# Kernel tuning notes

Measured on AMD Instinct MI355X. Metric: run time of the kernel, lower is better.

## Reference

```python
import jax, jax.numpy as jnp
import numpy as np

B, T, C = 2, 2048, 2048
N_HEAD, N_GROUP = 32, 8
HEAD_DIM = C // N_HEAD           # 64
HIG = N_HEAD // N_GROUP          # heads per group = 4


def setup_inputs() -> dict:
    key = jax.random.key(0)
    ks = jax.random.split(key, 8)
    s = 1.0 / np.sqrt(C)
    return {
        "q": jax.random.normal(ks[0], (B, T, C), jnp.float32),
        "k": jax.random.normal(ks[1], (B, T, C), jnp.float32),
        "v": jax.random.normal(ks[2], (B, T, C), jnp.float32),
        "Wq": jax.random.normal(ks[3], (C, C), jnp.float32) * s,
        "Wk": jax.random.normal(ks[4], (N_GROUP * HEAD_DIM, C), jnp.float32) * s,
        "Wv": jax.random.normal(ks[5], (N_GROUP * HEAD_DIM, C), jnp.float32) * s,
        "Wp": jax.random.normal(ks[6], (C, C), jnp.float32) * s,
        "bp": jax.random.normal(ks[7], (C,), jnp.float32) * s,
    }


def reference(q, k, v, Wq, Wk, Wv, Wp, bp):
    # Q projection -> (B, HIG, G, T, D); head h = i*G + g (row-major split of n_head)
    qp = (q @ Wq.T).reshape(B, T, N_HEAD, HEAD_DIM)
    qp = qp.transpose(0, 2, 1, 3).reshape(B, HIG, N_GROUP, T, HEAD_DIM)
    # K/V projections -> (B, G, T, D), shared across heads within a group
    kp = (k @ Wk.T).reshape(B, T, N_GROUP, HEAD_DIM).transpose(0, 2, 1, 3)
    vp = (v @ Wv.T).reshape(B, T, N_GROUP, HEAD_DIM).transpose(0, 2, 1, 3)
    scale = 1.0 / jnp.sqrt(jnp.asarray(HEAD_DIM, qp.dtype))
    scores = jnp.einsum('bigtd,bgsd->bigts', qp, kp) * scale  # (B,HIG,G,T,T)
    attn = jax.nn.softmax(scores, axis=-1)
    out = jnp.einsum('bigts,bgsd->bigtd', attn, vp)           # (B,HIG,G,T,D)
    out = out.reshape(B, N_HEAD, T, HEAD_DIM).transpose(0, 2, 1, 3).reshape(B, T, C)
    return out @ Wp.T + bp  # dropout is identity in eval mode
```

## Files before the change

### kernel.cpp

```cpp
#include <hip/hip_runtime.h>

#define DEVI __device__ __forceinline__

typedef __bf16 bf16_t;
typedef __bf16 bf16x8 __attribute__((ext_vector_type(8)));
typedef __bf16 bf16x4v __attribute__((ext_vector_type(4)));
typedef float f32x4 __attribute__((ext_vector_type(4)));

#define CSL 0.18033688011112042f

#if __has_builtin(__builtin_amdgcn_exp2f)
DEVI float fast_exp2(float x) { return __builtin_amdgcn_exp2f(x); }
#else
DEVI float fast_exp2(float x) {
  float r;
  asm volatile("v_exp_f32 %0, %1\n\ts_nop 1" : "=v"(r) : "v"(x));
  return r;
}
#endif

DEVI void async16(void* lds, const void* g) {
  __builtin_amdgcn_global_load_lds(
      (const __attribute__((address_space(1))) unsigned int*)g,
      (__attribute__((address_space(3))) unsigned int*)lds, 16, 0, 0);
}

__global__ __launch_bounds__(256) void cvt3(const float* __restrict__ a,
                                            const float* __restrict__ b,
                                            const float* __restrict__ c,
                                            bf16_t* __restrict__ da,
                                            bf16_t* __restrict__ db,
                                            bf16_t* __restrict__ dc, int n) {
  const float* s = (blockIdx.y == 0) ? a : (blockIdx.y == 1) ? b : c;
  bf16_t* d = (blockIdx.y == 0) ? da : (blockIdx.y == 1) ? db : dc;
  const int i = (blockIdx.x * 256 + threadIdx.x) * 4;
  if (i < n) {
    const float4 f = *(const float4*)(s + i);
    bf16x4v o;
    o.x = (bf16_t)f.x; o.y = (bf16_t)f.y; o.z = (bf16_t)f.z; o.w = (bf16_t)f.w;
    *(bf16x4v*)(d + i) = o;
  }
}
__global__ __launch_bounds__(256) void cvt2(const float* __restrict__ a,
                                            const float* __restrict__ b,
                                            bf16_t* __restrict__ da,
                                            bf16_t* __restrict__ db, int n) {
  const float* s = (blockIdx.y == 0) ? a : b;
  bf16_t* d = (blockIdx.y == 0) ? da : db;
  const int i = (blockIdx.x * 256 + threadIdx.x) * 4;
  if (i < n) {
    const float4 f = *(const float4*)(s + i);
    bf16x4v o;
    o.x = (bf16_t)f.x; o.y = (bf16_t)f.y; o.z = (bf16_t)f.z; o.w = (bf16_t)f.w;
    *(bf16x4v*)(d + i) = o;
  }
}

template<int MODE>
DEVI void gemm_core(const bf16_t* __restrict__ A, const bf16_t* __restrict__ W,
                    const float* __restrict__ bias, void* __restrict__ outv,
                    int N, int K, int bx, int by)
{
  __shared__ __align__(16) bf16_t Al[128 * 32];
  __shared__ __align__(16) bf16_t Bl[128 * 32];
  const int t = threadIdx.x;
  const int w = t >> 6, lane = t & 63;
  const int l15 = lane & 15, quad = lane >> 4;
  const int wm = (w >> 1) * 64, wn = (w & 1) * 64;
  const int m0 = by * 128, n0 = bx * 128;
  const int srow = t >> 2;
  const int skc = (t & 3) * 8;

  f32x4 acc[4][4] = {};

  for (int kk = 0; kk < K; kk += 32) {
    __syncthreads();
#pragma unroll
    for (int i = 0; i < 2; ++i) {
      async16(Al + i * 2048 + w * 512,
              A + (size_t)(m0 + i * 64 + srow) * K + kk + skc);
      async16(Bl + i * 2048 + w * 512,
              W + (size_t)(n0 + i * 64 + srow) * K + kk + skc);
    }
    __syncthreads();
    bf16x8 af[4], bfr[4];
#pragma unroll
    for (int x = 0; x < 4; ++x) {
      af[x]  = *(const bf16x8*)&Al[(wm + x * 16 + l15) * 32 + quad * 8];
      bfr[x] = *(const bf16x8*)&Bl[(wn + x * 16 + l15) * 32 + quad * 8];
    }
#pragma unroll
    for (int mt = 0; mt < 4; ++mt)
#pragma unroll
      for (int nt = 0; nt < 4; ++nt)
        acc[mt][nt] = __builtin_amdgcn_mfma_f32_16x16x32_bf16(af[mt], bfr[nt], acc[mt][nt], 0, 0, 0);
  }

#pragma unroll
  for (int mt = 0; mt < 4; ++mt) {
#pragma unroll
    for (int nt = 0; nt < 4; ++nt) {
      const int n = n0 + wn + nt * 16 + l15;
#pragma unroll
      for (int r = 0; r < 4; ++r) {
        const int m = m0 + wm + mt * 16 + quad * 4 + r;
        const float v = acc[mt][nt][r];
        if (MODE == 0) {
          ((bf16_t*)outv)[(size_t)m * N + n] = (bf16_t)v;
        } else if (MODE == 1) {
          ((float*)outv)[(size_t)m * N + n] = v + bias[n];
        } else if (MODE == 2) {
          ((bf16_t*)outv)[(size_t)(m >> 11) * (512 * 2048) + (size_t)n * 2048 + (m & 2047)] = (bf16_t)v;
        } else {
          ((bf16_t*)outv)[(size_t)m * N + n] = (bf16_t)(v * CSL);
        }
      }
    }
  }
}

__global__ __launch_bounds__(256) void gemm_scaled(const bf16_t* __restrict__ A,
                                                   const bf16_t* __restrict__ W,
                                                   bf16_t* __restrict__ out, int N, int K) {
  gemm_core<3>(A, W, nullptr, out, N, K, blockIdx.x, blockIdx.y);
}
__global__ __launch_bounds__(256) void gemm_bias_f32(const bf16_t* __restrict__ A,
                                                     const bf16_t* __restrict__ W,
                                                     const float* __restrict__ bias,
                                                     float* __restrict__ out, int N, int K) {
  gemm_core<1>(A, W, bias, out, N, K, blockIdx.x, blockIdx.y);
}
__global__ __launch_bounds__(256) void gemm_kv(const bf16_t* __restrict__ kin,
                                               const bf16_t* __restrict__ Wk,
                                               bf16_t* __restrict__ kp,
                                               const bf16_t* __restrict__ vin,
                                               const bf16_t* __restrict__ Wv,
                                               bf16_t* __restrict__ vt) {
  if (blockIdx.z == 0) gemm_core<0>(kin, Wk, nullptr, kp, 512, 2048, blockIdx.x, blockIdx.y);
  else                 gemm_core<2>(vin, Wv, nullptr, vt, 512, 2048, blockIdx.x, blockIdx.y);
}

__global__ __launch_bounds__(256) void attn_kernel(
    const bf16_t* __restrict__ Qp, const bf16_t* __restrict__ Kp,
    const bf16_t* __restrict__ Vt, bf16_t* __restrict__ O)
{
  __shared__ __align__(16) bf16_t Kl[64 * 64];
  __shared__ __align__(16) bf16_t Vl[64 * 64];
  __shared__ __align__(16) bf16_t Pl[4 * 32 * 64];

  const int t = threadIdx.x;
  const int w = t >> 6, lane = t & 63;
  const int l15 = lane & 15, quad = lane >> 4;
  const int h = blockIdx.y, b = blockIdx.z, g = h & 7;
  const int t0 = blockIdx.x * 128 + w * 32;

  const size_t qbase = (size_t)b * (2048u * 2048u) + (size_t)h * 64;
  const size_t kbase = (size_t)b * (2048u * 512u) + (size_t)g * 64;
  const size_t vbase = (size_t)b * (512u * 2048u) + (size_t)(g * 64) * 2048u;

  bf16x8 qf[2][2];
#pragma unroll
  for (int nt = 0; nt < 2; ++nt)
#pragma unroll
    for (int kc = 0; kc < 2; ++kc)
      qf[nt][kc] = *(const bf16x8*)&Qp[qbase + (size_t)(t0 + nt * 16 + l15) * 2048 + kc * 32 + quad * 8];

  f32x4 oacc[2][4] = {};
  float rs[2] = {0.f, 0.f};

  const int srow = t >> 3;
  const int sc8 = (t & 7) * 8;
  const int swz = (((t & 7) ^ (srow & 7)) << 3);
  const int xk = l15 & 7;
  const int xp = (l15 & 7) << 1;
  const int pbase = w << 11;

  for (int it = 0; it < 32; ++it) {
    const int s0 = it * 64;
    bf16x8 kreg[2], vreg[2];
#pragma unroll
    for (int i = 0; i < 2; ++i) {
      const int row = i * 32 + srow;
      kreg[i] = *(const bf16x8*)&Kp[kbase + (size_t)(s0 + row) * 512 + sc8];
      vreg[i] = *(const bf16x8*)&Vt[vbase + (size_t)row * 2048 + s0 + sc8];
    }
    __syncthreads();
#pragma unroll
    for (int i = 0; i < 2; ++i) {
      const int row = i * 32 + srow;
      *(bf16x8*)&Kl[(row << 6) + swz] = kreg[i];
      *(bf16x8*)&Vl[(row << 6) + swz] = vreg[i];
    }
    __syncthreads();

    f32x4 sacc[4][2] = {};
#pragma unroll
    for (int kc = 0; kc < 2; ++kc) {
#pragma unroll
      for (int kt = 0; kt < 4; ++kt) {
        bf16x8 kf = *(const bf16x8*)&Kl[((kt * 16 + l15) << 6) + (((kc * 4 + quad) ^ xk) << 3)];
#pragma unroll
        for (int nt = 0; nt < 2; ++nt)
          sacc[kt][nt] = __builtin_amdgcn_mfma_f32_16x16x32_bf16(kf, qf[nt][kc], sacc[kt][nt], 0, 0, 0);
      }
    }

#pragma unroll
    for (int nt = 0; nt < 2; ++nt) {
#pragma unroll
      for (int kt = 0; kt < 4; ++kt) {
        const float p0 = fast_exp2(sacc[kt][nt][0]);
        const float p1 = fast_exp2(sacc[kt][nt][1]);
        const float p2 = fast_exp2(sacc[kt][nt][2]);
        const float p3 = fast_exp2(sacc[kt][nt][3]);
        rs[nt] += (p0 + p1) + (p2 + p3);
        bf16x4v o;
        o.x = (bf16_t)p0; o.y = (bf16_t)p1; o.z = (bf16_t)p2; o.w = (bf16_t)p3;
        *(bf16x4v*)&Pl[pbase + ((nt * 16 + l15) << 6) + (((kt * 4 + quad) ^ xp) << 2)] = o;
      }
    }

#pragma unroll
    for (int kc = 0; kc < 2; ++kc) {
      bf16x8 pf[2];
#pragma unroll
      for (int mt = 0; mt < 2; ++mt)
        pf[mt] = *(const bf16x8*)&Pl[pbase + ((mt * 16 + l15) << 6) + (((kc * 8 + quad * 2) ^ xp) << 2)];
#pragma unroll
      for (int db = 0; db < 4; ++db) {
        bf16x8 vf = *(const bf16x8*)&Vl[((db * 16 + l15) << 6) + (((kc * 4 + quad) ^ xk) << 3)];
#pragma unroll
        for (int mt = 0; mt < 2; ++mt)
          oacc[mt][db] = __builtin_amdgcn_mfma_f32_16x16x32_bf16(pf[mt], vf, oacc[mt][db], 0, 0, 0);
      }
    }
  }

  float linv[2][4];
#pragma unroll
  for (int nt = 0; nt < 2; ++nt) {
    float rl = rs[nt];
    rl += __shfl_xor(rl, 16);
    rl += __shfl_xor(rl, 32);
#pragma unroll
    for (int r = 0; r < 4; ++r)
      linv[nt][r] = 1.0f / __shfl(rl, quad * 4 + r);
  }

#pragma unroll
  for (int mt = 0; mt < 2; ++mt)
#pragma unroll
    for (int db = 0; db < 4; ++db)
#pragma unroll
      for (int r = 0; r < 4; ++r) {
        const int tt = t0 + mt * 16 + quad * 4 + r;
        const int d = db * 16 + l15;
        O[((size_t)(b * 2048 + tt) * 32 + h) * 64 + d] = (bf16_t)(oacc[mt][db][r] * linv[mt][r]);
      }
}

extern "C" void kernel_launch(void* const* d_in, const int* in_sizes, int n_in,
                              void* d_out, int out_size, void* d_ws, size_t ws_size,
                              hipStream_t stream) {
  const float* q  = (const float*)d_in[0];
  const float* k  = (const float*)d_in[1];
  const float* v  = (const float*)d_in[2];
  const float* Wq = (const float*)d_in[3];
  const float* Wk = (const float*)d_in[4];
  const float* Wv = (const float*)d_in[5];
  const float* Wp = (const float*)d_in[6];
  const float* bp = (const float*)d_in[7];
  float* out = (float*)d_out;

  bf16_t* ws = (bf16_t*)d_ws;
  bf16_t* qb  = ws;
  bf16_t* kb  = ws +  8388608;
  bf16_t* vb  = ws + 16777216;
  bf16_t* Wqb = ws + 25165824;
  bf16_t* Wkb = ws + 29360128;
  bf16_t* Wvb = ws + 30408704;
  bf16_t* Wpb = ws + 31457280;
  bf16_t* Qp  = ws + 35651584;
  bf16_t* Kp  = ws + 44040192;
  bf16_t* Vt  = ws + 46137344;
  bf16_t* Ob  = qb;

  cvt3<<<dim3(8192, 3), 256, 0, stream>>>(q, k, v, qb, kb, vb, 8388608);
  cvt2<<<dim3(4096, 2), 256, 0, stream>>>(Wq, Wp, Wqb, Wpb, 4194304);
  cvt2<<<dim3(1024, 2), 256, 0, stream>>>(Wk, Wv, Wkb, Wvb, 1048576);

  gemm_scaled<<<dim3(16, 32), 256, 0, stream>>>(qb, Wqb, Qp, 2048, 2048);
  gemm_kv<<<dim3(4, 32, 2), 256, 0, stream>>>(kb, Wkb, Kp, vb, Wvb, Vt);
  attn_kernel<<<dim3(16, 32, 2), 256, 0, stream>>>(Qp, Kp, Vt, Ob);
  gemm_bias_f32<<<dim3(16, 32), 256, 0, stream>>>(Ob, Wpb, bp, out, 2048, 2048);
}
```

Baseline: 427.0 us.

## Load K/V fragments directly from global memory, dropping LDS staging and barriers

Each wave now reads its K and V MFMA fragments straight from global memory into registers, so the shared K/V tiles and both per-iteration __syncthreads are gone. Occupancy is hinted with launch_bounds(256,4), and s_setprio raises wave priority around the MFMA blocks. This removes block-wide synchronization and LDS traffic, but each of the four waves in a block now loads the same K/V data separately, which puts more load on L1/L2. The strided 16-byte global reads are also less coalesced than the earlier cooperative row loads.

Measured after the change: 712.0 us. 66.7% more time.

```diff
diff --git a/kernel.cpp b/kernel.cpp
--- a/kernel.cpp
+++ b/kernel.cpp
@@ -140,12 +140,10 @@
   else                 gemm_core<2>(vin, Wv, nullptr, vt, 512, 2048, blockIdx.x, blockIdx.y);
 }
 
-__global__ __launch_bounds__(256) void attn_kernel(
+__global__ __launch_bounds__(256, 4) void attn_kernel(
     const bf16_t* __restrict__ Qp, const bf16_t* __restrict__ Kp,
     const bf16_t* __restrict__ Vt, bf16_t* __restrict__ O)
 {
-  __shared__ __align__(16) bf16_t Kl[64 * 64];
-  __shared__ __align__(16) bf16_t Vl[64 * 64];
   __shared__ __align__(16) bf16_t Pl[4 * 32 * 64];
 
   const int t = threadIdx.x;
@@ -168,42 +166,41 @@
   f32x4 oacc[2][4] = {};
   float rs[2] = {0.f, 0.f};
 
-  const int srow = t >> 3;
-  const int sc8 = (t & 7) * 8;
-  const int swz = (((t & 7) ^ (srow & 7)) << 3);
-  const int xk = l15 & 7;
   const int xp = (l15 & 7) << 1;
   const int pbase = w << 11;
 
+  const bf16_t* kptr = Kp + kbase + (size_t)l15 * 512 + quad * 8;
+  const bf16_t* vptr = Vt + vbase + (size_t)l15 * 2048 + quad * 8;
+
   for (int it = 0; it < 32; ++it) {
     const int s0 = it * 64;
-    bf16x8 kreg[2], vreg[2];
-#pragma unroll
-    for (int i = 0; i < 2; ++i) {
-      const int row = i * 32 + srow;
-      kreg[i] = *(const bf16x8*)&Kp[kbase + (size_t)(s0 + row) * 512 + sc8];
-      vreg[i] = *(const bf16x8*)&Vt[vbase + (size_t)row * 2048 + s0 + sc8];
-    }
-    __syncthreads();
-#pragma unroll
-    for (int i = 0; i < 2; ++i) {
-      const int row = i * 32 + srow;
-      *(bf16x8*)&Kl[(row << 6) + swz] = kreg[i];
-      *(bf16x8*)&Vl[(row << 6) + swz] = vreg[i];
-    }
-    __syncthreads();
+
+    bf16x8 kf[2][4];
+#pragma unroll
+    for (int kc = 0; kc < 2; ++kc)
+#pragma unroll
+      for (int kt = 0; kt < 4; ++kt)
+        kf[kc][kt] = *(const bf16x8*)&kptr[(size_t)(s0 + kt * 16) * 512 + kc * 32];
+
+    bf16x8 vf[2][4];
+#pragma unroll
+    for (int kc = 0; kc < 2; ++kc)
+#pragma unroll
+      for (int db = 0; db < 4; ++db)
+        vf[kc][db] = *(const bf16x8*)&vptr[(size_t)(db * 16) * 2048 + s0 + kc * 32];
 
     f32x4 sacc[4][2] = {};
+    __builtin_amdgcn_s_setprio(1);
 #pragma unroll
     for (int kc = 0; kc < 2; ++kc) {
 #pragma unroll
       for (int kt = 0; kt < 4; ++kt) {
-        bf16x8 kf = *(const bf16x8*)&Kl[((kt * 16 + l15) << 6) + (((kc * 4 + quad) ^ xk) << 3)];
 #pragma unroll
         for (int nt = 0; nt < 2; ++nt)
-          sacc[kt][nt] = __builtin_amdgcn_mfma_f32_16x16x32_bf16(kf, qf[nt][kc], sacc[kt][nt], 0, 0, 0);
-      }
-    }
+          sacc[kt][nt] = __builtin_amdgcn_mfma_f32_16x16x32_bf16(kf[kc][kt], qf[nt][kc], sacc[kt][nt], 0, 0, 0);
+      }
+    }
+    __builtin_amdgcn_s_setprio(0);
 
 #pragma unroll
     for (int nt = 0; nt < 2; ++nt) {
@@ -226,13 +223,14 @@
 #pragma unroll
       for (int mt = 0; mt < 2; ++mt)
         pf[mt] = *(const bf16x8*)&Pl[pbase + ((mt * 16 + l15) << 6) + (((kc * 8 + quad * 2) ^ xp) << 2)];
+      __builtin_amdgcn_s_setprio(1);
 #pragma unroll
       for (int db = 0; db < 4; ++db) {
-        bf16x8 vf = *(const bf16x8*)&Vl[((db * 16 + l15) << 6) + (((kc * 4 + quad) ^ xk) << 3)];
 #pragma unroll
         for (int mt = 0; mt < 2; ++mt)
-          oacc[mt][db] = __builtin_amdgcn_mfma_f32_16x16x32_bf16(pf[mt], vf, oacc[mt][db], 0, 0, 0);
-      }
+          oacc[mt][db] = __builtin_amdgcn_mfma_f32_16x16x32_bf16(pf[mt], vf[kc][db], oacc[mt][db], 0, 0, 0);
+      }
+      __builtin_amdgcn_s_setprio(0);
     }
   }
 
```

## Double-buffer K/V tiles with async global-to-LDS loads in attention

Applied to the files above, without the earlier changes.

The attention kernel's K/V staging now uses two LDS buffers, filled with direct global-to-LDS async loads. The swizzle is applied on the source address, and the next tile is prefetched while the current one is computed. This removes the register round-trip and one barrier per iteration, so memory latency should hide behind the MFMA work. It also raises wave priority around MFMA issue and accumulates row sums as vectors. The P-tile swizzle is changed, with reads split into two 8-byte loads to avoid bank conflicts. Correctness depends on the async loads being waited on before the barrier, and doubled LDS may lower occupancy.

Result: no change. 429.5 us (+0.6%).

```diff
diff --git a/kernel.cpp b/kernel.cpp
--- a/kernel.cpp
+++ b/kernel.cpp
@@ -144,8 +144,8 @@
     const bf16_t* __restrict__ Qp, const bf16_t* __restrict__ Kp,
     const bf16_t* __restrict__ Vt, bf16_t* __restrict__ O)
 {
-  __shared__ __align__(16) bf16_t Kl[64 * 64];
-  __shared__ __align__(16) bf16_t Vl[64 * 64];
+  __shared__ __align__(16) bf16_t Kl[2][64 * 64];
+  __shared__ __align__(16) bf16_t Vl[2][64 * 64];
   __shared__ __align__(16) bf16_t Pl[4 * 32 * 64];
 
   const int t = threadIdx.x;
@@ -166,42 +166,47 @@
       qf[nt][kc] = *(const bf16x8*)&Qp[qbase + (size_t)(t0 + nt * 16 + l15) * 2048 + kc * 32 + quad * 8];
 
   f32x4 oacc[2][4] = {};
-  float rs[2] = {0.f, 0.f};
-
-  const int srow = t >> 3;
-  const int sc8 = (t & 7) * 8;
-  const int swz = (((t & 7) ^ (srow & 7)) << 3);
+  f32x4 rs4[2] = {};
+
   const int xk = l15 & 7;
-  const int xp = (l15 & 7) << 1;
+  const int xp = ((l15 & 7) << 1) | (l15 >> 3);
   const int pbase = w << 11;
 
+  const int lrow = lane >> 3;
+  const int lchk = (lane & 7) ^ lrow;
+  const bf16_t* ksrc = Kp + kbase + (size_t)(w * 8 + lrow) * 512 + lchk * 8;
+  const bf16_t* vsrc = Vt + vbase + (size_t)(w * 8 + lrow) * 2048 + lchk * 8;
+
+#pragma unroll
+  for (int i = 0; i < 2; ++i) {
+    async16(&Kl[0][(i * 32 + w * 8) * 64], ksrc + (size_t)(i * 32) * 512);
+    async16(&Vl[0][(i * 32 + w * 8) * 64], vsrc + (size_t)(i * 32) * 2048);
+  }
+
   for (int it = 0; it < 32; ++it) {
-    const int s0 = it * 64;
-    bf16x8 kreg[2], vreg[2];
-#pragma unroll
-    for (int i = 0; i < 2; ++i) {
-      const int row = i * 32 + srow;
-      kreg[i] = *(const bf16x8*)&Kp[kbase + (size_t)(s0 + row) * 512 + sc8];
-      vreg[i] = *(const bf16x8*)&Vt[vbase + (size_t)row * 2048 + s0 + sc8];
-    }
+    const int cur = it & 1;
     __syncthreads();
-#pragma unroll
-    for (int i = 0; i < 2; ++i) {
-      const int row = i * 32 + srow;
-      *(bf16x8*)&Kl[(row << 6) + swz] = kreg[i];
-      *(bf16x8*)&Vl[(row << 6) + swz] = vreg[i];
-    }
-    __syncthreads();
+
+    if (it < 31) {
+      const int s1 = (it + 1) * 64;
+#pragma unroll
+      for (int i = 0; i < 2; ++i) {
+        async16(&Kl[cur ^ 1][(i * 32 + w * 8) * 64], ksrc + (size_t)(s1 + i * 32) * 512);
+        async16(&Vl[cur ^ 1][(i * 32 + w * 8) * 64], vsrc + (size_t)(i * 32) * 2048 + s1);
+      }
+    }
 
     f32x4 sacc[4][2] = {};
 #pragma unroll
     for (int kc = 0; kc < 2; ++kc) {
 #pragma unroll
       for (int kt = 0; kt < 4; ++kt) {
-        bf16x8 kf = *(const bf16x8*)&Kl[((kt * 16 + l15) << 6) + (((kc * 4 + quad) ^ xk) << 3)];
+        bf16x8 kf = *(const bf16x8*)&Kl[cur][((kt * 16 + l15) << 6) + (((kc * 4 + quad) ^ xk) << 3)];
+        __builtin_amdgcn_s_setprio(1);
 #pragma unroll
         for (int nt = 0; nt < 2; ++nt)
           sacc[kt][nt] = __builtin_amdgcn_mfma_f32_16x16x32_bf16(kf, qf[nt][kc], sacc[kt][nt], 0, 0, 0);
+        __builtin_amdgcn_s_setprio(0);
       }
     }
 
@@ -213,7 +218,8 @@
         const float p1 = fast_exp2(sacc[kt][nt][1]);
         const float p2 = fast_exp2(sacc[kt][nt][2]);
         const float p3 = fast_exp2(sacc[kt][nt][3]);
-        rs[nt] += (p0 + p1) + (p2 + p3);
+        f32x4 pv; pv[0] = p0; pv[1] = p1; pv[2] = p2; pv[3] = p3;
+        rs4[nt] += pv;
         bf16x4v o;
         o.x = (bf16_t)p0; o.y = (bf16_t)p1; o.z = (bf16_t)p2; o.w = (bf16_t)p3;
         *(bf16x4v*)&Pl[pbase + ((nt * 16 + l15) << 6) + (((kt * 4 + quad) ^ xp) << 2)] = o;
@@ -224,14 +230,20 @@
     for (int kc = 0; kc < 2; ++kc) {
       bf16x8 pf[2];
 #pragma unroll
-      for (int mt = 0; mt < 2; ++mt)
-        pf[mt] = *(const bf16x8*)&Pl[pbase + ((mt * 16 + l15) << 6) + (((kc * 8 + quad * 2) ^ xp) << 2)];
+      for (int mt = 0; mt < 2; ++mt) {
+        const int rb = pbase + ((mt * 16 + l15) << 6);
+        bf16x4v plo = *(const bf16x4v*)&Pl[rb + (((kc * 8 + quad * 2)     ^ xp) << 2)];
+        bf16x4v phi = *(const bf16x4v*)&Pl[rb + (((kc * 8 + quad * 2 + 1) ^ xp) << 2)];
+        pf[mt] = __builtin_shufflevector(plo, phi, 0, 1, 2, 3, 4, 5, 6, 7);
+      }
 #pragma unroll
       for (int db = 0; db < 4; ++db) {
-        bf16x8 vf = *(const bf16x8*)&Vl[((db * 16 + l15) << 6) + (((kc * 4 + quad) ^ xk) << 3)];
+        bf16x8 vf = *(const bf16x8*)&Vl[cur][((db * 16 + l15) << 6) + (((kc * 4 + quad) ^ xk) << 3)];
+        __builtin_amdgcn_s_setprio(1);
 #pragma unroll
         for (int mt = 0; mt < 2; ++mt)
           oacc[mt][db] = __builtin_amdgcn_mfma_f32_16x16x32_bf16(pf[mt], vf, oacc[mt][db], 0, 0, 0);
+        __builtin_amdgcn_s_setprio(0);
       }
     }
   }
@@ -239,7 +251,7 @@
   float linv[2][4];
 #pragma unroll
   for (int nt = 0; nt < 2; ++nt) {
-    float rl = rs[nt];
+    float rl = (rs4[nt][0] + rs4[nt][1]) + (rs4[nt][2] + rs4[nt][3]);
     rl += __shfl_xor(rl, 16);
     rl += __shfl_xor(rl, 32);
 #pragma unroll
```
